# Kernel optimization log

Measured on AMD Instinct MI355X. Metric: run time of the kernel, lower is better.

The kernel has to match this reference:

```python
import jax, jax.numpy as jnp
from jax import lax
import numpy as np

HEADS = 4
BUCKET = 64
DEPTH = 4


def _conv(x, w, b):
    y = lax.conv_general_dilated(x, w, (1, 1), [(1, 1), (1, 1)],
                                 dimension_numbers=('NCHW', 'OIHW', 'NCHW'))
    return y + b[None, :, None, None]


def _convT(x, w, b):
    # torch ConvTranspose2d(k=4, s=2, p=1): flip kernel, swap io, lhs_dilation=2, pad k-1-p=2
    wk = jnp.flip(w, (2, 3)).transpose(1, 0, 2, 3)
    y = lax.conv_general_dilated(x, wk, (1, 1), [(2, 2), (2, 2)], lhs_dilation=(2, 2),
                                 dimension_numbers=('NCHW', 'OIHW', 'NCHW'))
    return y + b[None, :, None, None]


def _maxpool(x):
    return lax.reduce_window(x, -jnp.inf, lax.max, (1, 1, 2, 2), (1, 1, 2, 2), 'VALID')


def _ln(x, g, b):
    m = x.mean(-1, keepdims=True)
    v = ((x - m) ** 2).mean(-1, keepdims=True)
    return (x - m) / jnp.sqrt(v + 1e-5) * g + b


def _lsh_attention(x, Wqk, bqk, Wv, bv, Wo, bo, rot):
    # shared-QK LSH bucketed attention (single hash round), look-one-back chunks
    B, N, D = x.shape
    h, dh = HEADS, D // HEADS
    qk = (x @ Wqk + bqk).reshape(B, N, h, dh).transpose(0, 2, 1, 3)  # B h N dh
    v = (x @ Wv + bv).reshape(B, N, h, dh).transpose(0, 2, 1, 3)
    k = qk / (jnp.linalg.norm(qk, axis=-1, keepdims=True) + 1e-6)    # keys = normalized queries
    rotated = jnp.einsum('bhnd,hdr->bhnr', qk, rot)
    buckets = jnp.argmax(jnp.concatenate([rotated, -rotated], -1), -1)  # B h N
    ticker = jnp.arange(N)
    perm = jnp.argsort(buckets * N + ticker, axis=-1)  # stable sort by bucket
    inv_perm = jnp.argsort(perm, axis=-1)
    g = lambda t: jnp.take_along_axis(t, perm[..., None], axis=2)
    nc = N // BUCKET
    bq = g(qk).reshape(B, h, nc, BUCKET, dh)
    bk = g(k).reshape(B, h, nc, BUCKET, dh)
    bv_ = g(v).reshape(B, h, nc, BUCKET, dh)
    bk2 = jnp.concatenate([bk, jnp.roll(bk, 1, axis=2)], axis=3)   # look one chunk back
    bv2 = jnp.concatenate([bv_, jnp.roll(bv_, 1, axis=2)], axis=3)
    dots = jnp.einsum('bhcid,bhcjd->bhcij', bq, bk2) * (dh ** -0.5)
    spos = jnp.take_along_axis(jnp.broadcast_to(ticker, buckets.shape), perm, -1).reshape(B, h, nc, BUCKET)
    kpos = jnp.concatenate([spos, jnp.roll(spos, 1, axis=2)], axis=3)
    dots = jnp.where(spos[..., :, None] == kpos[..., None, :], -1e5, dots)  # mask self (q == k)
    attn = jax.nn.softmax(dots, -1)
    o = jnp.einsum('bhcij,bhcjd->bhcid', attn, bv2).reshape(B, h, N, dh)
    o = jnp.take_along_axis(o, inv_perm[..., None], axis=2)  # unsort
    return o.transpose(0, 2, 1, 3).reshape(B, N, D) @ Wo + bo


def _reformer(seq, ln1_g, ln1_b, Wqk, bqk, Wv, bv, Wo, bo, rot, ln2_g, ln2_b, Wff1, bff1, Wff2, bff2):
    for i in range(DEPTH):
        seq = seq + _lsh_attention(_ln(seq, ln1_g[i], ln1_b[i]), Wqk[i], bqk[i], Wv[i], bv[i], Wo[i], bo[i], rot[i])
        hdn = jax.nn.gelu(_ln(seq, ln2_g[i], ln2_b[i]) @ Wff1[i] + bff1[i])
        seq = seq + hdn @ Wff2[i] + bff2[i]
    return seq


def _forward(burst, conv1_w, conv1_b, conv2_w, conv2_b, conv3_w, conv3_b,
             ln1_g, ln1_b, Wqk, bqk, Wv, bv, Wo, bo, rot, ln2_g, ln2_b,
             Wff1, bff1, Wff2, bff2, up1_w, up1_b, dec1_w, dec1_b,
             up2_w, up2_b, dec2_w, dec2_b, out_w, out_b):
    B, T, C, H, W = burst.shape
    x = burst.reshape(B * T, C, H, W)
    e1 = jax.nn.relu(_conv(x, conv1_w, conv1_b))
    p1 = _maxpool(e1)
    e2 = jax.nn.relu(_conv(p1, conv2_w, conv2_b))
    p2 = _maxpool(e2)
    bm = jax.nn.relu(_conv(p2, conv3_w, conv3_b))
    D = bm.shape[1]
    Hq, Wq = H // 4, W // 4
    seq = bm.transpose(0, 2, 3, 1).reshape(B * T, Hq * Wq, D)
    seq = _reformer(seq, ln1_g, ln1_b, Wqk, bqk, Wv, bv, Wo, bo, rot, ln2_g, ln2_b, Wff1, bff1, Wff2, bff2)
    bm = seq.reshape(B * T, Hq, Wq, D).transpose(0, 3, 1, 2)
    d1 = _convT(bm, up1_w, up1_b)
    d1 = jax.nn.relu(_conv(jnp.concatenate([d1, e2], 1), dec1_w, dec1_b))
    d2 = _convT(d1, up2_w, up2_b)
    d2 = jax.nn.relu(_conv(jnp.concatenate([d2, e1], 1), dec2_w, dec2_b))
    sharp = jax.nn.sigmoid(_conv(d2, out_w, out_b))
    return sharp.reshape(B, T, C, H, W)[:, 0]


def setup_inputs() -> dict:
    key = jax.random.key(0)
    ks = jax.random.split(key, 20)
    s = 0.05
    n = lambda k, shape: jax.random.normal(k, shape, jnp.float32) * s
    inp = {}
    inp['burst'] = jax.random.uniform(ks[0], (1, 7, 3, 256, 256), jnp.float32)
    inp['conv1_w'] = n(ks[1], (64, 3, 3, 3)); inp['conv1_b'] = jnp.zeros((64,), jnp.float32)
    inp['conv2_w'] = n(ks[2], (128, 64, 3, 3)); inp['conv2_b'] = jnp.zeros((128,), jnp.float32)
    inp['conv3_w'] = n(ks[3], (256, 128, 3, 3)); inp['conv3_b'] = jnp.zeros((256,), jnp.float32)
    inp['ln1_g'] = jnp.ones((4, 256), jnp.float32); inp['ln1_b'] = jnp.zeros((4, 256), jnp.float32)
    inp['Wqk'] = n(ks[4], (4, 256, 256)); inp['bqk'] = jnp.zeros((4, 256), jnp.float32)
    inp['Wv'] = n(ks[5], (4, 256, 256)); inp['bv'] = jnp.zeros((4, 256), jnp.float32)
    inp['Wo'] = n(ks[6], (4, 256, 256)); inp['bo'] = jnp.zeros((4, 256), jnp.float32)
    inp['rot'] = jax.random.normal(ks[7], (4, 4, 64, 32), jnp.float32)  # depth, heads, d_head, n_buckets//2
    inp['ln2_g'] = jnp.ones((4, 256), jnp.float32); inp['ln2_b'] = jnp.zeros((4, 256), jnp.float32)
    inp['Wff1'] = n(ks[8], (4, 256, 1024)); inp['bff1'] = jnp.zeros((4, 1024), jnp.float32)
    inp['Wff2'] = n(ks[9], (4, 1024, 256)); inp['bff2'] = jnp.zeros((4, 256), jnp.float32)
    inp['up1_w'] = n(ks[10], (256, 128, 4, 4)); inp['up1_b'] = jnp.zeros((128,), jnp.float32)
    inp['dec1_w'] = n(ks[11], (128, 256, 3, 3)); inp['dec1_b'] = jnp.zeros((128,), jnp.float32)
    inp['up2_w'] = n(ks[12], (128, 64, 4, 4)); inp['up2_b'] = jnp.zeros((64,), jnp.float32)
    inp['dec2_w'] = n(ks[13], (64, 128, 3, 3)); inp['dec2_b'] = jnp.zeros((64,), jnp.float32)
    inp['out_w'] = n(ks[14], (3, 64, 3, 3)); inp['out_b'] = jnp.zeros((3,), jnp.float32)
    return inp


def reference(burst, conv1_w, conv1_b, conv2_w, conv2_b, conv3_w, conv3_b,
              ln1_g, ln1_b, Wqk, bqk, Wv, bv, Wo, bo, rot, ln2_g, ln2_b,
              Wff1, bff1, Wff2, bff2, up1_w, up1_b, dec1_w, dec1_b,
              up2_w, up2_b, dec2_w, dec2_b, out_w, out_b):
    return _forward(burst, conv1_w, conv1_b, conv2_w, conv2_b, conv3_w, conv3_b,
                    ln1_g, ln1_b, Wqk, bqk, Wv, bv, Wo, bo, rot, ln2_g, ln2_b,
                    Wff1, bff1, Wff2, bff2, up1_w, up1_b, dec1_w, dec1_b,
                    up2_w, up2_b, dec2_w, dec2_b, out_w, out_b)
```

## Files before the change

### kernel.cpp

```cpp
#include <hip/hip_runtime.h>
#include <hip/hip_bf16.h>
#include <math.h>

using short8  = __attribute__((ext_vector_type(8))) short;
using half8   = __attribute__((ext_vector_type(8))) _Float16;
using floatx4 = __attribute__((ext_vector_type(4))) float;

static __device__ __forceinline__ float gelu_f(float x) {
    float x3 = x * x * x;
    return 0.5f * x * (1.f + tanhf(0.7978845608028654f * (x + 0.044715f * x3)));
}
static __device__ __forceinline__ short f2h(float f) {
    _Float16 h = (_Float16)f;
    return __builtin_bit_cast(short, h);
}
static __device__ __forceinline__ short f2bf(float f) {
    unsigned u = __float_as_uint(f);
    u += 0x7fffu + ((u >> 16) & 1u);
    return (short)(u >> 16);
}
static __device__ __forceinline__ float bf2f(short s) {
    return __uint_as_float(((unsigned)(unsigned short)s) << 16);
}
struct bf3s { short a, b, c; };
static __device__ __forceinline__ bf3s split3(float v) {
    short c0 = f2bf(v); float r = v - bf2f(c0);
    short c1 = f2bf(r); r -= bf2f(c1);
    short c2 = f2bf(r);
    bf3s s; s.a = c0; s.b = c1; s.c = c2; return s;
}

template <int OCB>
__global__ __launch_bounds__(256) void conv1_nhwc_kernel(
    const float* __restrict__ in1, const float* __restrict__ w,
    const float* __restrict__ bias, float* __restrict__ out,
    short* __restrict__ outh, int H, int W, int OC)
{
    int tx = threadIdx.x, ty = threadIdx.y;
    int x = blockIdx.x * 16 + tx, y = blockIdx.y * 16 + ty;
    int oc0 = blockIdx.z * OCB;
    const int C = 3;
    float acc[OCB];
#pragma unroll
    for (int o = 0; o < OCB; ++o) acc[o] = 0.f;
    for (int ic = 0; ic < C; ++ic) {
        const float* src = in1 + (size_t)ic * H * W;
        float v[9];
#pragma unroll
        for (int ky = 0; ky < 3; ++ky) {
            int iy = y + ky - 1;
            bool okY = (iy >= 0) && (iy < H);
#pragma unroll
            for (int kx = 0; kx < 3; ++kx) {
                int ix = x + kx - 1;
                bool ok = okY && (ix >= 0) && (ix < W);
                v[ky * 3 + kx] = ok ? src[(size_t)iy * W + ix] : 0.f;
            }
        }
        const float* wp = w + ((size_t)oc0 * C + ic) * 9;
#pragma unroll
        for (int o = 0; o < OCB; ++o) {
            const float* wo = wp + (size_t)o * C * 9;
            acc[o] += v[0]*wo[0] + v[1]*wo[1] + v[2]*wo[2]
                    + v[3]*wo[3] + v[4]*wo[4] + v[5]*wo[5]
                    + v[6]*wo[6] + v[7]*wo[7] + v[8]*wo[8];
        }
    }
    size_t ob = ((size_t)y * W + x) * OC + oc0;
#pragma unroll
    for (int o = 0; o < OCB; ++o) {
        float r = fmaxf(acc[o] + bias[oc0 + o], 0.f);
        out[ob + o] = r;
        outh[ob + o] = f2h(r);
    }
}

__global__ __launch_bounds__(256) void maxpool1_bf3_kernel(
    const float* __restrict__ in, short* __restrict__ o0, short* __restrict__ o1,
    short* __restrict__ o2, int OW, int IW, int C)
{
    int idx = blockIdx.x * 256 + threadIdx.x;
    int g = idx % (C >> 2); int p = idx / (C >> 2);
    int x = p % OW; int y = p / OW;
    size_t base = ((size_t)(2 * y) * IW + 2 * x) * C + g * 4;
    float4 a = *(const float4*)(in + base);
    float4 b = *(const float4*)(in + base + C);
    float4 c = *(const float4*)(in + base + (size_t)IW * C);
    float4 d = *(const float4*)(in + base + (size_t)IW * C + C);
    float v[4];
    v[0] = fmaxf(fmaxf(a.x, b.x), fmaxf(c.x, d.x));
    v[1] = fmaxf(fmaxf(a.y, b.y), fmaxf(c.y, d.y));
    v[2] = fmaxf(fmaxf(a.z, b.z), fmaxf(c.z, d.z));
    v[3] = fmaxf(fmaxf(a.w, b.w), fmaxf(c.w, d.w));
    size_t o = (size_t)p * C + g * 4;
#pragma unroll
    for (int j = 0; j < 4; ++j) {
        bf3s s = split3(v[j]);
        o0[o + j] = s.a; o1[o + j] = s.b; o2[o + j] = s.c;
    }
}

__global__ __launch_bounds__(256) void maxpool2_bf3_kernel(
    const short* __restrict__ i0, const short* __restrict__ i1,
    const short* __restrict__ i2, short* __restrict__ o0, short* __restrict__ o1,
    short* __restrict__ o2, int OW, int IW, int C)
{
    int idx = blockIdx.x * 256 + threadIdx.x;
    int g = idx % (C >> 2); int p = idx / (C >> 2);
    int x = p % OW; int y = p / OW;
    float v[4] = {-1e30f, -1e30f, -1e30f, -1e30f};
#pragma unroll
    for (int dy = 0; dy < 2; ++dy)
#pragma unroll
        for (int dx = 0; dx < 2; ++dx) {
            size_t base = ((size_t)(2 * y + dy) * IW + 2 * x + dx) * C + g * 4;
#pragma unroll
            for (int j = 0; j < 4; ++j) {
                float u = bf2f(i0[base + j]) + bf2f(i1[base + j]) + bf2f(i2[base + j]);
                v[j] = fmaxf(v[j], u);
            }
        }
    size_t o = (size_t)p * C + g * 4;
#pragma unroll
    for (int j = 0; j < 4; ++j) {
        bf3s s = split3(v[j]);
        o0[o + j] = s.a; o1[o + j] = s.b; o2[o + j] = s.c;
    }
}

__global__ void pack_conv3_kernel(const float* __restrict__ w,
                                  short* __restrict__ B0, short* __restrict__ B1,
                                  short* __restrict__ B2, int C, int OC, int total)
{
    int t = blockIdx.x * 256 + threadIdx.x;
    if (t >= total) return;
    int lane = t & 63, fi = t >> 6;
    int NT = OC >> 4;
    int nt = fi % NT, kt = fi / NT;
    int cpt = C >> 5;
    int tap = kt / cpt, ct = kt % cpt;
    int c = ct * 32 + (lane >> 4) * 8;
    int oc = nt * 16 + (lane & 15);
    short8 v0, v1, v2;
#pragma unroll
    for (int j = 0; j < 8; ++j) {
        bf3s s = split3(w[((size_t)oc * C + c + j) * 9 + tap]);
        v0[j] = s.a; v1[j] = s.b; v2[j] = s.c;
    }
    ((short8*)B0)[t] = v0; ((short8*)B1)[t] = v1; ((short8*)B2)[t] = v2;
}

__global__ __launch_bounds__(256) void conv_bf3_kernel(
    const short* __restrict__ ia0, const short* __restrict__ ia1,
    const short* __restrict__ ia2,
    const short* __restrict__ B0, const short* __restrict__ B1,
    const short* __restrict__ B2, const float* __restrict__ bias,
    float* __restrict__ outf, short* __restrict__ o0, short* __restrict__ o1,
    short* __restrict__ o2, short* __restrict__ oh,
    int H, int W, int C, int OC)
{
    int tid = threadIdx.x, wave = tid >> 6, lane = tid & 63;
    int quad = lane >> 4, l16 = lane & 15;
    int x0 = blockIdx.x * 64, y = blockIdx.y, nt0 = blockIdx.z * 4;
    int cpt = C >> 5, NT = OC >> 4;
    const short8* b0p = (const short8*)B0;
    const short8* b1p = (const short8*)B1;
    const short8* b2p = (const short8*)B2;
    floatx4 aM[4] = {{0,0,0,0},{0,0,0,0},{0,0,0,0},{0,0,0,0}};
    floatx4 aC[4] = {{0,0,0,0},{0,0,0,0},{0,0,0,0},{0,0,0,0}};
    int xm = x0 + wave * 16 + l16;
    for (int ky = 0; ky < 3; ++ky) {
        int yy = y + ky - 1;
        bool rok = (yy >= 0) && (yy < H);
        for (int kx = 0; kx < 3; ++kx) {
            int xx = xm + kx - 1;
            bool ok = rok && (xx >= 0) && (xx < W);
            size_t pos = (size_t)yy * W + xx;
            int ktb = (ky * 3 + kx) * cpt;
            for (int ct = 0; ct < cpt; ++ct) {
                int cc = ct * 32 + quad * 8;
                short8 A0 = {0,0,0,0,0,0,0,0}, A1 = A0, A2 = A0;
                if (ok) {
                    A0 = *(const short8*)(ia0 + pos * C + cc);
                    A1 = *(const short8*)(ia1 + pos * C + cc);
                    A2 = *(const short8*)(ia2 + pos * C + cc);
                }
                size_t bi = ((size_t)(ktb + ct) * NT + nt0) * 64 + lane;
#pragma unroll
                for (int s = 0; s < 4; ++s) {
                    short8 w0 = b0p[bi + s * 64];
                    short8 w1 = b1p[bi + s * 64];
                    short8 w2 = b2p[bi + s * 64];
                    aM[s] = __builtin_amdgcn_mfma_f32_16x16x32_bf16(A0, w0, aM[s], 0, 0, 0);
                    aC[s] = __builtin_amdgcn_mfma_f32_16x16x32_bf16(A0, w1, aC[s], 0, 0, 0);
                    aC[s] = __builtin_amdgcn_mfma_f32_16x16x32_bf16(A1, w0, aC[s], 0, 0, 0);
                    aC[s] = __builtin_amdgcn_mfma_f32_16x16x32_bf16(A0, w2, aC[s], 0, 0, 0);
                    aC[s] = __builtin_amdgcn_mfma_f32_16x16x32_bf16(A1, w1, aC[s], 0, 0, 0);
                    aC[s] = __builtin_amdgcn_mfma_f32_16x16x32_bf16(A2, w0, aC[s], 0, 0, 0);
                }
            }
        }
    }
#pragma unroll
    for (int s = 0; s < 4; ++s) {
        int n = (nt0 + s) * 16 + l16;
        float bs = bias[n];
#pragma unroll
        for (int r = 0; r < 4; ++r) {
            int m = wave * 16 + quad * 4 + r;
            int x = x0 + m;
            float v = fmaxf(aM[s][r] + aC[s][r] + bs, 0.f);
            size_t o = ((size_t)y * W + x) * OC + n;
            if (outf) outf[o] = v;
            else {
                bf3s sp = split3(v);
                o0[o] = sp.a; o1[o] = sp.b; o2[o] = sp.c;
                oh[o] = f2h(v);
            }
        }
    }
}

__global__ __launch_bounds__(256) void ln_bf3_kernel(
    const float* __restrict__ x, const float* __restrict__ g,
    const float* __restrict__ b, short* __restrict__ y0,
    short* __restrict__ y1, short* __restrict__ y2)
{
    int wave = threadIdx.x >> 6, lane = threadIdx.x & 63;
    int n = blockIdx.x * 4 + wave;
    const float* xr = x + (size_t)n * 256;
    float4 v = *(const float4*)(xr + lane * 4);
    float s = v.x + v.y + v.z + v.w;
#pragma unroll
    for (int m = 1; m < 64; m <<= 1) s += __shfl_xor(s, m);
    float mean = s * (1.f / 256.f);
    float cx = v.x - mean, cy = v.y - mean, cz = v.z - mean, cw = v.w - mean;
    float q = cx * cx + cy * cy + cz * cz + cw * cw;
#pragma unroll
    for (int m = 1; m < 64; m <<= 1) q += __shfl_xor(q, m);
    float rstd = rsqrtf(q * (1.f / 256.f) + 1e-5f);
    float4 gv = *(const float4*)(g + lane * 4);
    float4 bv = *(const float4*)(b + lane * 4);
    float o[4];
    o[0] = cx * rstd * gv.x + bv.x;
    o[1] = cy * rstd * gv.y + bv.y;
    o[2] = cz * rstd * gv.z + bv.z;
    o[3] = cw * rstd * gv.w + bv.w;
    size_t ob = (size_t)n * 256 + lane * 4;
#pragma unroll
    for (int j = 0; j < 4; ++j) {
        bf3s sp = split3(o[j]);
        y0[ob + j] = sp.a; y1[ob + j] = sp.b; y2[ob + j] = sp.c;
    }
}

__global__ __launch_bounds__(256) void bucketn_kernel(
    const float* __restrict__ qk, const float* __restrict__ rot,
    int* __restrict__ buckets, float* __restrict__ knrm)
{
    int t = blockIdx.x * 256 + threadIdx.x;
    int h = t >> 12, n = t & 4095;
    const float* q = qk + (size_t)n * 256 + h * 64;
    const float* R = rot + (size_t)h * 2048;
    float acc[32];
#pragma unroll
    for (int r = 0; r < 32; ++r) acc[r] = 0.f;
    float s2 = 0.f;
    for (int d = 0; d < 64; ++d) {
        float qd = q[d];
        s2 += qd * qd;
        const float* Rd = R + d * 32;
#pragma unroll
        for (int r = 0; r < 32; ++r) acc[r] += qd * Rd[r];
    }
    knrm[t] = 1.f / (sqrtf(s2) + 1e-6f);
    float bvv = acc[0]; int best = 0;
#pragma unroll
    for (int j = 1; j < 64; ++j) {
        float val = (j < 32) ? acc[j] : -acc[j - 32];
        if (val > bvv) { bvv = val; best = j; }
    }
    buckets[t] = best;
}

__global__ __launch_bounds__(256) void lsh_sort_kernel(
    const int* __restrict__ buckets, int* __restrict__ perm)
{
    int h = blockIdx.x;
    const int* bk = buckets + h * 4096;
    __shared__ unsigned long long mask[64][64];
    __shared__ int counts[64];
    __shared__ int offsets[64];
    __shared__ int wpre[64][64];
    int tid = threadIdx.x, wave = tid >> 6, lane = tid & 63;
    for (int w = wave * 16; w < wave * 16 + 16; ++w) {
        int bl = bk[w * 64 + lane];
        for (int b = 0; b < 64; ++b) {
            unsigned long long m = __ballot(bl == b);
            if (lane == b) mask[b][w] = m;
        }
    }
    __syncthreads();
    if (tid < 64) {
        int c = 0;
        for (int w = 0; w < 64; ++w) c += __popcll(mask[tid][w]);
        counts[tid] = c;
    }
    __syncthreads();
    if (tid == 0) {
        int a = 0;
        for (int b = 0; b < 64; ++b) { offsets[b] = a; a += counts[b]; }
    }
    __syncthreads();
    for (int b = wave * 16; b < wave * 16 + 16; ++b) {
        int c = __popcll(mask[b][lane]);
        int incl = c;
#pragma unroll
        for (int off = 1; off < 64; off <<= 1) {
            int nb = __shfl_up(incl, off);
            if (lane >= off) incl += nb;
        }
        wpre[b][lane] = incl - c + offsets[b];
    }
    __syncthreads();
    for (int i = tid; i < 4096; i += 256) {
        int b = bk[i]; int w = i >> 6; int l = i & 63;
        unsigned long long below = mask[b][w] & ((1ull << l) - 1ull);
        int pos = wpre[b][w] + __popcll(below);
        perm[h * 4096 + pos] = i;
    }
}

__global__ __launch_bounds__(256) void attn_kernel(
    const float* __restrict__ qk, const float* __restrict__ vv,
    const float* __restrict__ knrm, const int* __restrict__ perm,
    short* __restrict__ o0, short* __restrict__ o1, short* __restrict__ o2)
{
    __shared__ float ks[128 * 64];
    __shared__ float dotsT[128 * 32];
    __shared__ float pmax[8][32];
    __shared__ float psum[8][32];
    int c = blockIdx.x, h = blockIdx.y, rh = blockIdx.z;
    int tid = threadIdx.x;
    const int* pm = perm + h * 4096;
    int cm = (c + 63) & 63;
    {
        int jr = tid >> 1, hf = tid & 1;
        int sk = (jr < 64) ? (c * 64 + jr) : (cm * 64 + (jr - 64));
        int nk = pm[sk];
        float sc = knrm[h * 4096 + nk];
        const float* src = qk + (size_t)nk * 256 + h * 64 + hf * 32;
        float* dst = ks + jr * 64 + hf * 32;
#pragma unroll
        for (int d = 0; d < 32; d += 4) {
            float4 v = *(const float4*)(src + d);
            v.x *= sc; v.y *= sc; v.z *= sc; v.w *= sc;
            *(float4*)(dst + d) = v;
        }
    }
    __syncthreads();
    int rr = tid & 31, jq = tid >> 5;
    int r = rh * 32 + rr;
    int nq = pm[c * 64 + r];
    float mx = -1e30f;
    {
        float qreg[64];
        const float* src = qk + (size_t)nq * 256 + h * 64;
#pragma unroll
        for (int d = 0; d < 64; d += 4) {
            float4 v = *(const float4*)(src + d);
            qreg[d] = v.x; qreg[d + 1] = v.y; qreg[d + 2] = v.z; qreg[d + 3] = v.w;
        }
        for (int jj = 0; jj < 16; ++jj) {
            int j = jq * 16 + jj;
            const float* kr = ks + j * 64;
            float dot = 0.f;
#pragma unroll
            for (int d = 0; d < 64; d += 4) {
                float4 kv = *(const float4*)(kr + d);
                dot += qreg[d] * kv.x + qreg[d + 1] * kv.y
                     + qreg[d + 2] * kv.z + qreg[d + 3] * kv.w;
            }
            int sk = (j < 64) ? (c * 64 + j) : (cm * 64 + (j - 64));
            int nk = pm[sk];
            dot = (nk == nq) ? -1e5f : dot * 0.125f;
            dotsT[j * 32 + rr] = dot;
            mx = fmaxf(mx, dot);
        }
    }
    pmax[jq][rr] = mx;
    __syncthreads();
    float gmax = pmax[0][rr];
#pragma unroll
    for (int g = 1; g < 8; ++g) gmax = fmaxf(gmax, pmax[g][rr]);
    float ss = 0.f;
    for (int jj = 0; jj < 16; ++jj) {
        int j = jq * 16 + jj;
        float e = expf(dotsT[j * 32 + rr] - gmax);
        dotsT[j * 32 + rr] = e;
        ss += e;
    }
    psum[jq][rr] = ss;
    {
        int jr = tid >> 1, hf = tid & 1;
        int sk = (jr < 64) ? (c * 64 + jr) : (cm * 64 + (jr - 64));
        int nk = pm[sk];
        const float* src = vv + (size_t)nk * 256 + h * 64 + hf * 32;
        float* dst = ks + jr * 64 + hf * 32;
#pragma unroll
        for (int d = 0; d < 32; d += 4)
            *(float4*)(dst + d) = *(const float4*)(src + d);
    }
    __syncthreads();
    float tot = psum[0][rr];
#pragma unroll
    for (int g = 1; g < 8; ++g) tot += psum[g][rr];
    float inv = 1.f / tot;
    float acc[8] = {0.f, 0.f, 0.f, 0.f, 0.f, 0.f, 0.f, 0.f};
    for (int j = 0; j < 128; ++j) {
        float a = dotsT[j * 32 + rr];
        const float* vr = ks + j * 64 + jq * 8;
        float4 v0 = *(const float4*)(vr);
        float4 v1 = *(const float4*)(vr + 4);
        acc[0] += a * v0.x; acc[1] += a * v0.y; acc[2] += a * v0.z; acc[3] += a * v0.w;
        acc[4] += a * v1.x; acc[5] += a * v1.y; acc[6] += a * v1.z; acc[7] += a * v1.w;
    }
    size_t ob = (size_t)nq * 256 + h * 64 + jq * 8;
#pragma unroll
    for (int d = 0; d < 8; ++d) {
        bf3s sp = split3(acc[d] * inv);
        o0[ob + d] = sp.a; o1[ob + d] = sp.b; o2[ob + d] = sp.c;
    }
}

static __device__ __forceinline__ void pack_one(
    const float* __restrict__ W, short* __restrict__ B0, short* __restrict__ B1,
    short* __restrict__ B2, int N, int t)
{
    int lane = t & 63, fi = t >> 6;
    int NT = N >> 4;
    int nt = fi % NT, kt = fi / NT;
    int n = nt * 16 + (lane & 15);
    int k0 = kt * 32 + (lane >> 4) * 8;
    short8 v0, v1, v2;
#pragma unroll
    for (int j = 0; j < 8; ++j) {
        bf3s s = split3(W[(size_t)(k0 + j) * N + n]);
        v0[j] = s.a; v1[j] = s.b; v2[j] = s.c;
    }
    ((short8*)B0)[t] = v0; ((short8*)B1)[t] = v1; ((short8*)B2)[t] = v2;
}

__global__ void pack_layer_kernel(
    const float* __restrict__ Wqk, const float* __restrict__ Wv,
    const float* __restrict__ Wo, const float* __restrict__ Wff1,
    const float* __restrict__ Wff2,
    short* q0, short* q1, short* q2, short* v0, short* v1, short* v2,
    short* o0, short* o1, short* o2, short* f10, short* f11, short* f12,
    short* f20, short* f21, short* f22)
{
    int t = blockIdx.x * 256 + threadIdx.x;
    if (t < 8192)       pack_one(Wqk, q0, q1, q2, 256, t);
    else if (t < 16384) pack_one(Wv, v0, v1, v2, 256, t - 8192);
    else if (t < 24576) pack_one(Wo, o0, o1, o2, 256, t - 16384);
    else if (t < 57344) pack_one(Wff1, f10, f11, f12, 1024, t - 24576);
    else if (t < 90112) pack_one(Wff2, f20, f21, f22, 256, t - 57344);
}

static __device__ __forceinline__ void gemm_bf3_core(
    const short* __restrict__ A0, const short* __restrict__ A1,
    const short* __restrict__ A2,
    const short* __restrict__ B0, const short* __restrict__ B1,
    const short* __restrict__ B2, const float* __restrict__ bias,
    float* __restrict__ Cf, short* __restrict__ D0, short* __restrict__ D1,
    short* __restrict__ D2, short* __restrict__ Dh,
    int N, int K, int act, int resid, int bx, int by)
{
    int tid = threadIdx.x, wave = tid >> 6, lane = tid & 63;
    int quad = lane >> 4, l16 = lane & 15;
    int m0 = by * 64 + wave * 16;
    int NT = N >> 4, nt0 = bx * 2;
    size_t arow = (size_t)(m0 + l16) * K + quad * 8;
    const short8* b0p = (const short8*)B0;
    const short8* b1p = (const short8*)B1;
    const short8* b2p = (const short8*)B2;
    floatx4 aM0 = {0,0,0,0}, aM1 = {0,0,0,0};
    floatx4 aC10 = {0,0,0,0}, aC11 = {0,0,0,0};
    floatx4 aC20 = {0,0,0,0}, aC21 = {0,0,0,0};
    int KT = K >> 5;
    size_t bi0 = (size_t)nt0 * 64 + lane;
    short8 a0 = *(const short8*)(A0 + arow);
    short8 a1 = *(const short8*)(A1 + arow);
    short8 a2 = *(const short8*)(A2 + arow);
    short8 w00 = b0p[bi0], w01 = b1p[bi0], w02 = b2p[bi0];
    short8 w10 = b0p[bi0 + 64], w11 = b1p[bi0 + 64], w12 = b2p[bi0 + 64];
    for (int kt = 0; kt < KT; ++kt) {
        short8 na0 = {}, na1 = {}, na2 = {};
        short8 nw00 = {}, nw01 = {}, nw02 = {}, nw10 = {}, nw11 = {}, nw12 = {};
        if (kt + 1 < KT) {
            size_t ar = arow + (size_t)(kt + 1) * 32;
            na0 = *(const short8*)(A0 + ar);
            na1 = *(const short8*)(A1 + ar);
            na2 = *(const short8*)(A2 + ar);
            size_t nbi = ((size_t)(kt + 1) * NT + nt0) * 64 + lane;
            nw00 = b0p[nbi]; nw01 = b1p[nbi]; nw02 = b2p[nbi];
            nw10 = b0p[nbi + 64]; nw11 = b1p[nbi + 64]; nw12 = b2p[nbi + 64];
        }
        aM0  = __builtin_amdgcn_mfma_f32_16x16x32_bf16(a0, w00, aM0, 0, 0, 0);
        aM1  = __builtin_amdgcn_mfma_f32_16x16x32_bf16(a0, w10, aM1, 0, 0, 0);
        aC10 = __builtin_amdgcn_mfma_f32_16x16x32_bf16(a0, w01, aC10, 0, 0, 0);
        aC11 = __builtin_amdgcn_mfma_f32_16x16x32_bf16(a0, w11, aC11, 0, 0, 0);
        aC20 = __builtin_amdgcn_mfma_f32_16x16x32_bf16(a1, w00, aC20, 0, 0, 0);
        aC21 = __builtin_amdgcn_mfma_f32_16x16x32_bf16(a1, w10, aC21, 0, 0, 0);
        aC10 = __builtin_amdgcn_mfma_f32_16x16x32_bf16(a0, w02, aC10, 0, 0, 0);
        aC11 = __builtin_amdgcn_mfma_f32_16x16x32_bf16(a0, w12, aC11, 0, 0, 0);
        aC20 = __builtin_amdgcn_mfma_f32_16x16x32_bf16(a1, w01, aC20, 0, 0, 0);
        aC21 = __builtin_amdgcn_mfma_f32_16x16x32_bf16(a1, w11, aC21, 0, 0, 0);
        aC10 = __builtin_amdgcn_mfma_f32_16x16x32_bf16(a2, w00, aC10, 0, 0, 0);
        aC11 = __builtin_amdgcn_mfma_f32_16x16x32_bf16(a2, w10, aC11, 0, 0, 0);
        a0 = na0; a1 = na1; a2 = na2;
        w00 = nw00; w01 = nw01; w02 = nw02;
        w10 = nw10; w11 = nw11; w12 = nw12;
    }
    floatx4 aM[2] = {aM0, aM1};
    floatx4 c1[2] = {aC10, aC11};
    floatx4 c2[2] = {aC20, aC21};
#pragma unroll
    for (int s = 0; s < 2; ++s) {
        int n = (nt0 + s) * 16 + l16;
        float bs = bias[n];
#pragma unroll
        for (int r = 0; r < 4; ++r) {
            int m = m0 + quad * 4 + r;
            float v = aM[s][r] + (c1[s][r] + c2[s][r]) + bs;
            if (act == 1) v = gelu_f(v);
            size_t o = (size_t)m * N + n;
            if (D0) {
                bf3s sp = split3(v);
                D0[o] = sp.a; D1[o] = sp.b; D2[o] = sp.c;
            } else {
                if (resid) v += Cf[o];
                Cf[o] = v;
                if (Dh) Dh[o] = f2h(v);
            }
        }
    }
}

__global__ __launch_bounds__(256) void gemm_bf3_kernel(
    const short* A0, const short* A1, const short* A2,
    const short* B0, const short* B1, const short* B2,
    const float* bias, float* Cf, short* D0, short* D1, short* D2, short* Dh,
    int N, int K, int act, int resid)
{
    gemm_bf3_core(A0, A1, A2, B0, B1, B2, bias, Cf, D0, D1, D2, Dh,
                  N, K, act, resid, blockIdx.x, blockIdx.y);
}

__global__ __launch_bounds__(256) void gemm_qkv_bf3_kernel(
    const short* A0, const short* A1, const short* A2,
    const short* Q0, const short* Q1, const short* Q2,
    const float* qb, float* Cq,
    const short* V0, const short* V1, const short* V2,
    const float* vb, float* Cv, int K)
{
    int side = blockIdx.x >> 3;
    gemm_bf3_core(A0, A1, A2, side ? V0 : Q0, side ? V1 : Q1, side ? V2 : Q2,
                  side ? vb : qb, side ? Cv : Cq, nullptr, nullptr, nullptr,
                  nullptr, 256, K, 0, 0, blockIdx.x & 7, blockIdx.y);
}

__global__ void pack_conv_kernel(const float* __restrict__ w, short* __restrict__ Bp,
                                 int C, int OC, int NT, int total)
{
    int t = blockIdx.x * 256 + threadIdx.x;
    if (t >= total) return;
    int lane = t & 63, fi = t >> 6;
    int nt = fi % NT, kt = fi / NT;
    int cpt = C >> 5;
    int tap = kt / cpt, ct = kt % cpt;
    int c = ct * 32 + (lane >> 4) * 8;
    int oc = nt * 16 + (lane & 15);
    short8 v;
#pragma unroll
    for (int j = 0; j < 8; ++j) {
        float f = (oc < OC) ? w[((size_t)oc * C + c + j) * 9 + tap] : 0.f;
        v[j] = f2h(f);
    }
    ((short8*)Bp)[t] = v;
}

__global__ void pack_convt_kernel(const float* __restrict__ w, short* __restrict__ Bp,
                                  int IC, int OC, int total)
{
    int t = blockIdx.x * 256 + threadIdx.x;
    if (t >= total) return;
    int lane = t & 63, fi = t >> 6;
    int NT = OC >> 4, cpt = IC >> 5, KT4 = 4 * cpt;
    int nt = fi % NT, r = fi / NT;
    int kt = r % KT4, pz = r / KT4;
    int py = pz >> 1, px = pz & 1;
    int t4 = kt / cpt, ct = kt % cpt;
    int ty = t4 >> 1, tx = t4 & 1;
    int ky = py ? (2 * ty) : (1 + 2 * ty);
    int kx = px ? (2 * tx) : (1 + 2 * tx);
    int ic = ct * 32 + (lane >> 4) * 8;
    int oc = nt * 16 + (lane & 15);
    short8 v;
#pragma unroll
    for (int j = 0; j < 8; ++j)
        v[j] = f2h(w[(((size_t)(ic + j) * OC + oc) * 4 + ky) * 4 + kx]);
    ((short8*)Bp)[t] = v;
}

__global__ __launch_bounds__(256) void conv_mfma_kernel(
    const short* __restrict__ in1, int C1, const short* __restrict__ in2, int C2,
    const short* __restrict__ Bp, const float* __restrict__ bias,
    short* __restrict__ outb, int H, int W, int OC)
{
    int tid = threadIdx.x, wave = tid >> 6, lane = tid & 63;
    int quad = lane >> 4, l16 = lane & 15;
    int x0 = blockIdx.x * 64, y = blockIdx.y, nt0 = blockIdx.z * 4;
    int C = C1 + C2, cpt = C >> 5, NT = OC >> 4;
    const half8* bp = (const half8*)Bp;
    floatx4 acc[4] = {{0,0,0,0},{0,0,0,0},{0,0,0,0},{0,0,0,0}};
    int xm = x0 + wave * 16 + l16;
    for (int ky = 0; ky < 3; ++ky) {
        int yy = y + ky - 1;
        bool rok = (yy >= 0) && (yy < H);
        for (int kx = 0; kx < 3; ++kx) {
            int xx = xm + kx - 1;
            bool ok = rok && (xx >= 0) && (xx < W);
            size_t pos = (size_t)yy * W + xx;
            int ktb = (ky * 3 + kx) * cpt;
            for (int ct = 0; ct < cpt; ++ct) {
                int cc = ct * 32 + quad * 8;
                half8 a = {};
                if (ok) {
                    const short* src = (cc < C1) ? (in1 + pos * C1 + cc)
                                                 : (in2 + pos * C2 + (cc - C1));
                    a = *(const half8*)src;
                }
                size_t bi = ((size_t)(ktb + ct) * NT + nt0) * 64 + lane;
#pragma unroll
                for (int s = 0; s < 4; ++s)
                    acc[s] = __builtin_amdgcn_mfma_f32_16x16x32_f16(a, bp[bi + s * 64], acc[s], 0, 0, 0);
            }
        }
    }
#pragma unroll
    for (int s = 0; s < 4; ++s) {
        int n = (nt0 + s) * 16 + l16;
        float bs = bias[n];
#pragma unroll
        for (int r = 0; r < 4; ++r) {
            int m = wave * 16 + quad * 4 + r;
            int x = x0 + m;
            float v = fmaxf(acc[s][r] + bs, 0.f);
            outb[((size_t)y * W + x) * OC + n] = f2h(v);
        }
    }
}

__global__ __launch_bounds__(256) void convt_mfma_kernel(
    const short* __restrict__ in, int IC, const short* __restrict__ Bp,
    const float* __restrict__ bias, short* __restrict__ outb, int IH, int IW, int OC)
{
    int tid = threadIdx.x, wave = tid >> 6, lane = tid & 63;
    int quad = lane >> 4, l16 = lane & 15;
    int pz = blockIdx.z & 3, nt0 = (blockIdx.z >> 2) * 4;
    int py = pz >> 1, px = pz & 1;
    int a0 = blockIdx.y, b0 = blockIdx.x * 64;
    int cpt = IC >> 5, NT = OC >> 4, KT4 = 4 * cpt;
    const half8* bp = (const half8*)Bp;
    floatx4 acc[4] = {{0,0,0,0},{0,0,0,0},{0,0,0,0},{0,0,0,0}};
    int bm = b0 + wave * 16 + l16;
    for (int ty = 0; ty < 2; ++ty) {
        int iy = a0 + (py ? (1 - ty) : (-ty));
        bool rok = (iy >= 0) && (iy < IH);
        for (int tx = 0; tx < 2; ++tx) {
            int ix = bm + (px ? (1 - tx) : (-tx));
            bool ok = rok && (ix >= 0) && (ix < IW);
            size_t pos = (size_t)iy * IW + ix;
            int ktb = (ty * 2 + tx) * cpt;
            for (int ct = 0; ct < cpt; ++ct) {
                int cc = ct * 32 + quad * 8;
                half8 a = {};
                if (ok) a = *(const half8*)(in + pos * IC + cc);
                size_t bi = ((size_t)(pz * KT4 + ktb + ct) * NT + nt0) * 64 + lane;
#pragma unroll
                for (int s = 0; s < 4; ++s)
                    acc[s] = __builtin_amdgcn_mfma_f32_16x16x32_f16(a, bp[bi + s * 64], acc[s], 0, 0, 0);
            }
        }
    }
    int OW = IW * 2;
    int oy = 2 * a0 + py;
#pragma unroll
    for (int s = 0; s < 4; ++s) {
        int n = (nt0 + s) * 16 + l16;
        float bs = bias[n];
#pragma unroll
        for (int r = 0; r < 4; ++r) {
            int m = wave * 16 + quad * 4 + r;
            int ox = 2 * (b0 + m) + px;
            outb[((size_t)oy * OW + ox) * OC + n] = f2h(acc[s][r] + bs);
        }
    }
}

__global__ __launch_bounds__(256) void convout_mfma_kernel(
    const short* __restrict__ in, const short* __restrict__ Bp,
    const float* __restrict__ bias, float* __restrict__ out, int H, int W)
{
    int tid = threadIdx.x, wave = tid >> 6, lane = tid & 63;
    int quad = lane >> 4, l16 = lane & 15;
    int x0 = blockIdx.x * 64, y = blockIdx.y;
    const int C = 64, cpt = 2;
    const half8* bp = (const half8*)Bp;
    floatx4 acc = {0,0,0,0};
    int xm = x0 + wave * 16 + l16;
    for (int ky = 0; ky < 3; ++ky) {
        int yy = y + ky - 1;
        bool rok = (yy >= 0) && (yy < H);
        for (int kx = 0; kx < 3; ++kx) {
            int xx = xm + kx - 1;
            bool ok = rok && (xx >= 0) && (xx < W);
            size_t pos = (size_t)yy * W + xx;
            int ktb = (ky * 3 + kx) * cpt;
#pragma unroll
            for (int ct = 0; ct < cpt; ++ct) {
                int cc = ct * 32 + quad * 8;
                half8 a = {};
                if (ok) a = *(const half8*)(in + pos * C + cc);
                acc = __builtin_amdgcn_mfma_f32_16x16x32_f16(
                          a, bp[(size_t)(ktb + ct) * 64 + lane], acc, 0, 0, 0);
            }
        }
    }
    int oc = l16;
    if (oc < 3) {
        float bs = bias[oc];
#pragma unroll
        for (int r = 0; r < 4; ++r) {
            int m = wave * 16 + quad * 4 + r;
            int x = x0 + m;
            float v = acc[r] + bs;
            out[(size_t)oc * H * W + (size_t)y * W + x] = 1.f / (1.f + expf(-v));
        }
    }
}

extern "C" void kernel_launch(void* const* d_in, const int* in_sizes, int n_in,
                              void* d_out, int out_size, void* d_ws, size_t ws_size,
                              hipStream_t stream)
{
    const float* burst   = (const float*)d_in[0];
    const float* conv1_w = (const float*)d_in[1];  const float* conv1_b = (const float*)d_in[2];
    const float* conv2_w = (const float*)d_in[3];  const float* conv2_b = (const float*)d_in[4];
    const float* conv3_w = (const float*)d_in[5];  const float* conv3_b = (const float*)d_in[6];
    const float* ln1_g   = (const float*)d_in[7];  const float* ln1_b   = (const float*)d_in[8];
    const float* Wqk     = (const float*)d_in[9];  const float* bqk     = (const float*)d_in[10];
    const float* Wv      = (const float*)d_in[11]; const float* bvv     = (const float*)d_in[12];
    const float* Wo      = (const float*)d_in[13]; const float* bo      = (const float*)d_in[14];
    const float* rot     = (const float*)d_in[15];
    const float* ln2_g   = (const float*)d_in[16]; const float* ln2_b   = (const float*)d_in[17];
    const float* Wff1    = (const float*)d_in[18]; const float* bff1    = (const float*)d_in[19];
    const float* Wff2    = (const float*)d_in[20]; const float* bff2    = (const float*)d_in[21];
    const float* up1_w   = (const float*)d_in[22]; const float* up1_b   = (const float*)d_in[23];
    const float* dec1_w  = (const float*)d_in[24]; const float* dec1_b  = (const float*)d_in[25];
    const float* up2_w   = (const float*)d_in[26]; const float* up2_b   = (const float*)d_in[27];
    const float* dec2_w  = (const float*)d_in[28]; const float* dec2_b  = (const float*)d_in[29];
    const float* out_w   = (const float*)d_in[30]; const float* out_b   = (const float*)d_in[31];

    float* ws = (float*)d_ws;
    short* e1h = (short*)(ws + 0);
    short* e2h = (short*)(ws + 2097152);
    float* seq = ws + 3145728;
    float* qkb = ws + 4194304;
    float* vvb = ws + 5242880;
    float* knb = ws + 6291456;
    int* buckets = (int*)(ws + 6307840);
    int* perm    = (int*)(ws + 6324224);
    short* xn0 = (short*)(ws + 6340608);
    short* xn1 = (short*)(ws + 6864896);
    short* xn2 = (short*)(ws + 7389184);
    short* hdn0 = (short*)(ws + 7913472);
    short* hdn1 = (short*)(ws + 10010624);
    short* hdn2 = (short*)(ws + 12107776);
    short* pqk0 = (short*)(ws + 14204928); short* pqk1 = (short*)(ws + 14237696); short* pqk2 = (short*)(ws + 14270464);
    short* pv0  = (short*)(ws + 14303232); short* pv1  = (short*)(ws + 14336000); short* pv2  = (short*)(ws + 14368768);
    short* po0  = (short*)(ws + 14401536); short* po1  = (short*)(ws + 14434304); short* po2  = (short*)(ws + 14467072);
    short* pf10 = (short*)(ws + 14499840); short* pf11 = (short*)(ws + 14630912); short* pf12 = (short*)(ws + 14761984);
    short* pf20 = (short*)(ws + 14893056); short* pf21 = (short*)(ws + 15024128); short* pf22 = (short*)(ws + 15155200);
    short* pdec1 = (short*)(ws + 15286272);
    short* pdec2 = (short*)(ws + 15433728);
    short* pout  = (short*)(ws + 15470592);
    short* pup1  = (short*)(ws + 15475200);
    short* pup2  = (short*)(ws + 15737344);
    float* e1f = ws + 7913472;
    short* p1_0 = (short*)(ws + 12107776); short* p1_1 = (short*)(ws + 12632064); short* p1_2 = (short*)(ws + 13156352);
    short* p2_0 = (short*)(ws + 13680640); short* p2_1 = (short*)(ws + 13942784); short* p2_2 = (short*)(ws + 14204928);
    short* pc2_0 = (short*)(ws + 14467072); short* pc2_1 = (short*)(ws + 14503936); short* pc2_2 = (short*)(ws + 14540800);
    short* pc3_0 = (short*)(ws + 14577664); short* pc3_1 = (short*)(ws + 14725120); short* pc3_2 = (short*)(ws + 14872576);
    short* e2_0 = (short*)(ws + 4194304); short* e2_1 = (short*)(ws + 5242880); short* e2_2 = (short*)(ws + 6291456);
    short* seqh = (short*)(ws + 7913472);
    short* d1   = (short*)(ws + 8437760);
    short* d1c  = (short*)(ws + 9486336);
    short* d2   = (short*)(ws + 10534912);
    short* d2c  = (short*)(ws + 12632064);

    dim3 b16(16, 16);

    pack_conv3_kernel<<<36, 256, 0, stream>>>(conv2_w, pc2_0, pc2_1, pc2_2, 64, 128, 9216);
    pack_conv3_kernel<<<144, 256, 0, stream>>>(conv3_w, pc3_0, pc3_1, pc3_2, 128, 256, 36864);
    pack_conv_kernel<<<144, 256, 0, stream>>>(dec1_w, pdec1, 256, 128, 8, 36864);
    pack_conv_kernel<<<36, 256, 0, stream>>>(dec2_w, pdec2, 128, 64, 4, 9216);
    pack_conv_kernel<<<5, 256, 0, stream>>>(out_w, pout, 64, 3, 1, 1152);
    pack_convt_kernel<<<256, 256, 0, stream>>>(up1_w, pup1, 256, 128, 65536);
    pack_convt_kernel<<<64, 256, 0, stream>>>(up2_w, pup2, 128, 64, 16384);

    conv1_nhwc_kernel<8><<<dim3(16, 16, 8), b16, 0, stream>>>(
        burst, conv1_w, conv1_b, e1f, e1h, 256, 256, 64);
    maxpool1_bf3_kernel<<<1024, 256, 0, stream>>>(e1f, p1_0, p1_1, p1_2, 128, 256, 64);
    conv_bf3_kernel<<<dim3(2, 128, 2), 256, 0, stream>>>(
        p1_0, p1_1, p1_2, pc2_0, pc2_1, pc2_2, conv2_b,
        nullptr, e2_0, e2_1, e2_2, e2h, 128, 128, 64, 128);
    maxpool2_bf3_kernel<<<512, 256, 0, stream>>>(
        e2_0, e2_1, e2_2, p2_0, p2_1, p2_2, 64, 128, 128);
    conv_bf3_kernel<<<dim3(1, 64, 4), 256, 0, stream>>>(
        p2_0, p2_1, p2_2, pc3_0, pc3_1, pc3_2, conv3_b,
        seq, nullptr, nullptr, nullptr, nullptr, 64, 64, 128, 256);

    for (int i = 0; i < 4; ++i) {
        pack_layer_kernel<<<352, 256, 0, stream>>>(
            Wqk + i * 65536, Wv + i * 65536, Wo + i * 65536,
            Wff1 + i * 262144, Wff2 + i * 262144,
            pqk0, pqk1, pqk2, pv0, pv1, pv2, po0, po1, po2,
            pf10, pf11, pf12, pf20, pf21, pf22);
        ln_bf3_kernel<<<1024, 256, 0, stream>>>(seq, ln1_g + i * 256, ln1_b + i * 256,
                                                xn0, xn1, xn2);
        gemm_qkv_bf3_kernel<<<dim3(16, 64), 256, 0, stream>>>(
            xn0, xn1, xn2, pqk0, pqk1, pqk2, bqk + i * 256, qkb,
            pv0, pv1, pv2, bvv + i * 256, vvb, 256);
        bucketn_kernel<<<64, 256, 0, stream>>>(qkb, rot + i * 8192, buckets, knb);
        lsh_sort_kernel<<<4, 256, 0, stream>>>(buckets, perm);
        attn_kernel<<<dim3(64, 4, 2), 256, 0, stream>>>(qkb, vvb, knb, perm, xn0, xn1, xn2);
        gemm_bf3_kernel<<<dim3(8, 64), 256, 0, stream>>>(
            xn0, xn1, xn2, po0, po1, po2, bo + i * 256, seq,
            nullptr, nullptr, nullptr, nullptr, 256, 256, 0, 1);
        ln_bf3_kernel<<<1024, 256, 0, stream>>>(seq, ln2_g + i * 256, ln2_b + i * 256,
                                                xn0, xn1, xn2);
        gemm_bf3_kernel<<<dim3(32, 64), 256, 0, stream>>>(
            xn0, xn1, xn2, pf10, pf11, pf12, bff1 + i * 1024, nullptr,
            hdn0, hdn1, hdn2, nullptr, 1024, 256, 1, 0);
        gemm_bf3_kernel<<<dim3(8, 64), 256, 0, stream>>>(
            hdn0, hdn1, hdn2, pf20, pf21, pf22, bff2 + i * 256, seq,
            nullptr, nullptr, nullptr, (i == 3) ? seqh : nullptr, 256, 1024, 0, 1);
    }

    convt_mfma_kernel<<<dim3(1, 64, 8), 256, 0, stream>>>(
        seqh, 256, pup1, up1_b, d1, 64, 64, 128);
    conv_mfma_kernel<<<dim3(2, 128, 2), 256, 0, stream>>>(
        d1, 128, e2h, 128, pdec1, dec1_b, d1c, 128, 128, 128);
    convt_mfma_kernel<<<dim3(2, 128, 4), 256, 0, stream>>>(
        d1c, 128, pup2, up2_b, d2, 128, 128, 64);
    conv_mfma_kernel<<<dim3(4, 256, 1), 256, 0, stream>>>(
        d2, 64, e1h, 64, pdec2, dec2_b, d2c, 256, 256, 64);
    convout_mfma_kernel<<<dim3(4, 256), 256, 0, stream>>>(
        d2c, pout, out_b, (float*)d_out, 256, 256);
}
```

Before: 1.321 ms.

## Stage conv3 input halo in LDS and widen LSH bucket/sort launches

The bf16x3 conv kernel now loads a 3-row by 66-column halo tile of each input split plane into shared memory, 64 channels at a time. It then reads the A fragments from LDS for all nine taps instead of issuing repeated global loads. The MFMA work is regrouped per input plane, which means the weight fragments are reloaded up to three times and extra barriers are added. Separately, bucketn is launched with 64-thread blocks across more blocks, and lsh_sort uses 1024 threads per block, to spread these small kernels over more compute units and waves.

```diff
diff --git a/kernel.cpp b/kernel.cpp
--- a/kernel.cpp
+++ b/kernel.cpp
@@ -159,6 +159,7 @@
     short* __restrict__ o2, short* __restrict__ oh,
     int H, int W, int C, int OC)
 {
+    __shared__ short sa[3 * 66 * 68];
     int tid = threadIdx.x, wave = tid >> 6, lane = tid & 63;
     int quad = lane >> 4, l16 = lane & 15;
     int x0 = blockIdx.x * 64, y = blockIdx.y, nt0 = blockIdx.z * 4;
@@ -166,37 +167,51 @@
     const short8* b0p = (const short8*)B0;
     const short8* b1p = (const short8*)B1;
     const short8* b2p = (const short8*)B2;
+    const short* ia[3] = {ia0, ia1, ia2};
     floatx4 aM[4] = {{0,0,0,0},{0,0,0,0},{0,0,0,0},{0,0,0,0}};
     floatx4 aC[4] = {{0,0,0,0},{0,0,0,0},{0,0,0,0},{0,0,0,0}};
-    int xm = x0 + wave * 16 + l16;
-    for (int ky = 0; ky < 3; ++ky) {
-        int yy = y + ky - 1;
-        bool rok = (yy >= 0) && (yy < H);
-        for (int kx = 0; kx < 3; ++kx) {
-            int xx = xm + kx - 1;
-            bool ok = rok && (xx >= 0) && (xx < W);
-            size_t pos = (size_t)yy * W + xx;
-            int ktb = (ky * 3 + kx) * cpt;
-            for (int ct = 0; ct < cpt; ++ct) {
-                int cc = ct * 32 + quad * 8;
-                short8 A0 = {0,0,0,0,0,0,0,0}, A1 = A0, A2 = A0;
-                if (ok) {
-                    A0 = *(const short8*)(ia0 + pos * C + cc);
-                    A1 = *(const short8*)(ia1 + pos * C + cc);
-                    A2 = *(const short8*)(ia2 + pos * C + cc);
-                }
-                size_t bi = ((size_t)(ktb + ct) * NT + nt0) * 64 + lane;
-#pragma unroll
-                for (int s = 0; s < 4; ++s) {
-                    short8 w0 = b0p[bi + s * 64];
-                    short8 w1 = b1p[bi + s * 64];
-                    short8 w2 = b2p[bi + s * 64];
-                    aM[s] = __builtin_amdgcn_mfma_f32_16x16x32_bf16(A0, w0, aM[s], 0, 0, 0);
-                    aC[s] = __builtin_amdgcn_mfma_f32_16x16x32_bf16(A0, w1, aC[s], 0, 0, 0);
-                    aC[s] = __builtin_amdgcn_mfma_f32_16x16x32_bf16(A1, w0, aC[s], 0, 0, 0);
-                    aC[s] = __builtin_amdgcn_mfma_f32_16x16x32_bf16(A0, w2, aC[s], 0, 0, 0);
-                    aC[s] = __builtin_amdgcn_mfma_f32_16x16x32_bf16(A1, w1, aC[s], 0, 0, 0);
-                    aC[s] = __builtin_amdgcn_mfma_f32_16x16x32_bf16(A2, w0, aC[s], 0, 0, 0);
+    int xl = wave * 16 + l16;
+    for (int p = 0; p < 3; ++p) {
+        const short* src_p = ia[p];
+        for (int c0 = 0; c0 < C; c0 += 64) {
+            __syncthreads();
+            for (int i = tid; i < 3 * 66 * 8; i += 256) {
+                int ch8 = i & 7; int rem = i >> 3;
+                int xx = rem % 66; int rr = rem / 66;
+                int gy = y + rr - 1, gx = x0 + xx - 1;
+                short8 v = {0,0,0,0,0,0,0,0};
+                if (gy >= 0 && gy < H && gx >= 0 && gx < W)
+                    v = *(const short8*)(src_p + ((size_t)gy * W + gx) * C + c0 + ch8 * 8);
+                *(short8*)(sa + (rr * 66 + xx) * 68 + ch8 * 8) = v;
+            }
+            __syncthreads();
+            for (int ky = 0; ky < 3; ++ky) {
+                for (int kx = 0; kx < 3; ++kx) {
+                    int ktb = (ky * 3 + kx) * cpt + (c0 >> 5);
+#pragma unroll
+                    for (int ct2 = 0; ct2 < 2; ++ct2) {
+                        short8 A = *(const short8*)(
+                            sa + (ky * 66 + xl + kx) * 68 + ct2 * 32 + quad * 8);
+                        size_t bi = ((size_t)(ktb + ct2) * NT + nt0) * 64 + lane;
+                        if (p == 0) {
+#pragma unroll
+                            for (int s = 0; s < 4; ++s) {
+                                aM[s] = __builtin_amdgcn_mfma_f32_16x16x32_bf16(A, b0p[bi + s * 64], aM[s], 0, 0, 0);
+                                aC[s] = __builtin_amdgcn_mfma_f32_16x16x32_bf16(A, b1p[bi + s * 64], aC[s], 0, 0, 0);
+                                aC[s] = __builtin_amdgcn_mfma_f32_16x16x32_bf16(A, b2p[bi + s * 64], aC[s], 0, 0, 0);
+                            }
+                        } else if (p == 1) {
+#pragma unroll
+                            for (int s = 0; s < 4; ++s) {
+                                aC[s] = __builtin_amdgcn_mfma_f32_16x16x32_bf16(A, b0p[bi + s * 64], aC[s], 0, 0, 0);
+                                aC[s] = __builtin_amdgcn_mfma_f32_16x16x32_bf16(A, b1p[bi + s * 64], aC[s], 0, 0, 0);
+                            }
+                        } else {
+#pragma unroll
+                            for (int s = 0; s < 4; ++s)
+                                aC[s] = __builtin_amdgcn_mfma_f32_16x16x32_bf16(A, b0p[bi + s * 64], aC[s], 0, 0, 0);
+                        }
+                    }
                 }
             }
         }
@@ -254,11 +269,11 @@
     }
 }
 
-__global__ __launch_bounds__(256) void bucketn_kernel(
+__global__ __launch_bounds__(64) void bucketn_kernel(
     const float* __restrict__ qk, const float* __restrict__ rot,
     int* __restrict__ buckets, float* __restrict__ knrm)
 {
-    int t = blockIdx.x * 256 + threadIdx.x;
+    int t = blockIdx.x * 64 + threadIdx.x;
     int h = t >> 12, n = t & 4095;
     const float* q = qk + (size_t)n * 256 + h * 64;
     const float* R = rot + (size_t)h * 2048;
@@ -283,7 +298,7 @@
     buckets[t] = best;
 }
 
-__global__ __launch_bounds__(256) void lsh_sort_kernel(
+__global__ __launch_bounds__(1024) void lsh_sort_kernel(
     const int* __restrict__ buckets, int* __restrict__ perm)
 {
     int h = blockIdx.x;
@@ -293,7 +308,7 @@
     __shared__ int offsets[64];
     __shared__ int wpre[64][64];
     int tid = threadIdx.x, wave = tid >> 6, lane = tid & 63;
-    for (int w = wave * 16; w < wave * 16 + 16; ++w) {
+    for (int w = wave * 4; w < wave * 4 + 4; ++w) {
         int bl = bk[w * 64 + lane];
         for (int b = 0; b < 64; ++b) {
             unsigned long long m = __ballot(bl == b);
@@ -312,7 +327,7 @@
         for (int b = 0; b < 64; ++b) { offsets[b] = a; a += counts[b]; }
     }
     __syncthreads();
-    for (int b = wave * 16; b < wave * 16 + 16; ++b) {
+    for (int b = wave * 4; b < wave * 4 + 4; ++b) {
         int c = __popcll(mask[b][lane]);
         int incl = c;
 #pragma unroll
@@ -323,7 +338,7 @@
         wpre[b][lane] = incl - c + offsets[b];
     }
     __syncthreads();
-    for (int i = tid; i < 4096; i += 256) {
+    for (int i = tid; i < 4096; i += 1024) {
         int b = bk[i]; int w = i >> 6; int l = i & 63;
         unsigned long long below = mask[b][w] & ((1ull << l) - 1ull);
         int pos = wpre[b][w] + __popcll(below);
@@ -843,8 +858,8 @@
         gemm_qkv_bf3_kernel<<<dim3(16, 64), 256, 0, stream>>>(
             xn0, xn1, xn2, pqk0, pqk1, pqk2, bqk + i * 256, qkb,
             pv0, pv1, pv2, bvv + i * 256, vvb, 256);
-        bucketn_kernel<<<64, 256, 0, stream>>>(qkb, rot + i * 8192, buckets, knb);
-        lsh_sort_kernel<<<4, 256, 0, stream>>>(buckets, perm);
+        bucketn_kernel<<<256, 64, 0, stream>>>(qkb, rot + i * 8192, buckets, knb);
+        lsh_sort_kernel<<<4, 1024, 0, stream>>>(buckets, perm);
         attn_kernel<<<dim3(64, 4, 2), 256, 0, stream>>>(qkb, vvb, knb, perm, xn0, xn1, xn2);
         gemm_bf3_kernel<<<dim3(8, 64), 256, 0, stream>>>(
             xn0, xn1, xn2, po0, po1, po2, bo + i * 256, seq,
```

Result: faster. 1.203 ms (-8.9%).
